# Kernel tuning notes

Hardware: AMD Instinct MI355X
Metric: run time of the kernel (lower is better)

Reference implementation:

```python
import jax, jax.numpy as jnp
import numpy as np
from jax import lax

MD = 4  # max displacement -> 9x9 = 81 correlation channels
NEG_SLOPE = 0.1


def leaky(x):
    return jnp.where(x >= 0, x, NEG_SLOPE * x)


def conv3x3(x, w):
    # NCHW conv, stride 1, padding 1, no bias
    return lax.conv_general_dilated(x, w, (1, 1), 'SAME',
                                    dimension_numbers=('NCHW', 'OIHW', 'NCHW'))


def upsample2x_bilinear(x):
    B, C, H, W = x.shape
    # matches torch F.interpolate(mode='bilinear', align_corners=False)
    return jax.image.resize(x, (B, C, 2 * H, 2 * W), method='bilinear')


def softsplat_average(inp, flow):
    """Forward-warp inp by flow with bilinear splatting, 'average' mode.
    inp: [B,C,H,W], flow: [B,2,H,W] (flow[:,0]=x disp, flow[:,1]=y disp)."""
    B, C, H, W = inp.shape
    val = jnp.concatenate([inp, jnp.ones((B, 1, H, W), inp.dtype)], axis=1)  # [B,C+1,H,W]
    gy, gx = jnp.meshgrid(jnp.arange(H, dtype=inp.dtype), jnp.arange(W, dtype=inp.dtype), indexing='ij')
    fx = gx[None] + flow[:, 0]  # [B,H,W] target x
    fy = gy[None] + flow[:, 1]  # [B,H,W] target y

    x0 = jnp.floor(fx)
    y0 = jnp.floor(fy)
    wx1 = fx - x0
    wy1 = fy - y0
    wx0 = 1.0 - wx1
    wy0 = 1.0 - wy1
    ix0 = x0.astype(jnp.int32)
    iy0 = y0.astype(jnp.int32)

    corners = [(ix0, iy0, wx0 * wy0), (ix0 + 1, iy0, wx1 * wy0),
               (ix0, iy0 + 1, wx0 * wy1), (ix0 + 1, iy0 + 1, wx1 * wy1)]

    def splat_one(val_b, corner_data):
        # val_b: [C+1,H,W]
        v = val_b.reshape(C + 1, H * W)
        out = jnp.zeros((C + 1, H * W), val_b.dtype)
        for ix, iy, w in corner_data:
            valid = (ix >= 0) & (ix < W) & (iy >= 0) & (iy < H)
            idx = jnp.clip(iy, 0, H - 1) * W + jnp.clip(ix, 0, W - 1)
            wv = jnp.where(valid, w, 0.0).reshape(H * W)
            out = out.at[:, idx.reshape(H * W)].add(v * wv[None, :])
        return out.reshape(C + 1, H, W)

    out = jax.vmap(splat_one)(val, [(c[0], c[1], c[2]) for c in corners])
    norm = out[:, -1:]
    norm = jnp.where(norm == 0.0, 1.0, norm)
    return out[:, :-1] / norm


def correlation(f0, f1):
    """PWC-style local cost volume, 9x9 window, mean over channels. [B,81,H,W]."""
    B, C, H, W = f0.shape
    f1p = jnp.pad(f1, ((0, 0), (0, 0), (MD, MD), (MD, MD)))
    vols = []
    for dy in range(2 * MD + 1):
        for dx in range(2 * MD + 1):
            shifted = f1p[:, :, dy:dy + H, dx:dx + W]
            vols.append(jnp.mean(f0 * shifted, axis=1))
    return jnp.stack(vols, axis=1)


def flow_compute(x, W1, W2, W3, W4, W5, W6, W7):
    h = conv3x3(x, W1)
    h = conv3x3(h, W2)
    h = conv3x3(h, W3)
    h = leaky(h)
    h = conv3x3(h, W4)
    h = conv3x3(h, W5)
    h = conv3x3(h, W6)
    h = conv3x3(h, W7)
    return leaky(h)


def setup_inputs() -> dict:
    key = jax.random.key(0)
    ks = jax.random.split(key, 12)
    B, C, H, W = 8, 32, 192, 320
    inp = {
        'feature_0': jax.random.normal(ks[0], (B, C, H, W), jnp.float32),
        'feature_1': jax.random.normal(ks[1], (B, C, H, W), jnp.float32),
        'bi_flow_previous': jax.random.normal(ks[2], (B, 4, H // 2, W // 2), jnp.float32),
        'forward_temporal_feature': jax.random.normal(ks[3], (B, C, H, W), jnp.float32),
        'backward_temporal_feature': jax.random.normal(ks[4], (B, C, H, W), jnp.float32),
        'W1': jax.random.normal(ks[5], (2 * C, 2 * C + 81, 3, 3), jnp.float32) * 0.05,
        'W2': jax.random.normal(ks[6], (2 * C, 2 * C, 3, 3), jnp.float32) * 0.05,
        'W3': jax.random.normal(ks[7], (2 * C, 2 * C, 3, 3), jnp.float32) * 0.05,
        'W4': jax.random.normal(ks[8], (C, 2 * C, 3, 3), jnp.float32) * 0.05,
        'W5': jax.random.normal(ks[9], (C, C, 3, 3), jnp.float32) * 0.05,
        'W6': jax.random.normal(ks[10], (C // 2, C, 3, 3), jnp.float32) * 0.05,
        'W7': jax.random.normal(ks[11], (2, C // 2, 3, 3), jnp.float32) * 0.05,
    }
    return inp


def reference(feature_0, feature_1, bi_flow_previous, forward_temporal_feature,
              backward_temporal_feature, W1, W2, W3, W4, W5, W6, W7):
    bi_flow = upsample2x_bilinear(bi_flow_previous) * 2.0  # [B,4,H,W]
    warped0 = softsplat_average(feature_0, bi_flow[:, :2])
    warped1 = softsplat_average(feature_1, bi_flow[:, 2:])
    volume = leaky(correlation(warped0, warped1))  # [B,81,H,W]
    ws = (W1, W2, W3, W4, W5, W6, W7)
    delta_f = flow_compute(jnp.concatenate([warped0, forward_temporal_feature, volume], axis=1), *ws)
    delta_b = flow_compute(jnp.concatenate([warped1, backward_temporal_feature, volume], axis=1), *ws)
    return bi_flow + jnp.concatenate([delta_f, delta_b], axis=1)
```

## Files before the change

kernel.cpp:

```cpp
#include <hip/hip_runtime.h>

#define IMH 192
#define IMW 320
#define HW_ (IMH * IMW)
#define BB 8
#define FC 32
#define GR 8
#define CCH 224

typedef unsigned short ushortT;
typedef __attribute__((ext_vector_type(8))) short short8;
typedef __attribute__((ext_vector_type(4))) float f32x4;

union FragU { uint4 u; short8 s8; };

__device__ __forceinline__ ushortT f2bf(float x) {
    union { float f; unsigned u; } v; v.f = x;
    unsigned r = v.u + 0x7FFF + ((v.u >> 16) & 1);
    return (ushortT)(r >> 16);
}
__device__ __forceinline__ float lk(float v) { return (v >= 0.f) ? v : 0.1f * v; }

__global__ __launch_bounds__(256) void upsample_k(const float* __restrict__ in,
                                                  float* __restrict__ out) {
    int gid = blockIdx.x * 256 + threadIdx.x;
    const int total = BB * 4 * IMH * IMW;
    if (gid >= total) return;
    int ox = gid % IMW;
    int t  = gid / IMW;
    int oy = t % IMH;
    int bc = t / IMH;
    const int Hin = IMH / 2, Win = IMW / 2;
    float sy = oy * 0.5f - 0.25f;
    float sx = ox * 0.5f - 0.25f;
    float fy = floorf(sy), fx = floorf(sx);
    float ty_ = sy - fy, tx_ = sx - fx;
    int y0 = (int)fy, x0 = (int)fx;
    int y1 = y0 + 1, x1 = x0 + 1;
    y0 = max(0, min(Hin - 1, y0)); y1 = max(0, min(Hin - 1, y1));
    x0 = max(0, min(Win - 1, x0)); x1 = max(0, min(Win - 1, x1));
    const float* p = in + (long)bc * Hin * Win;
    float v00 = p[y0 * Win + x0], v01 = p[y0 * Win + x1];
    float v10 = p[y1 * Win + x0], v11 = p[y1 * Win + x1];
    float v = (1.f - ty_) * ((1.f - tx_) * v00 + tx_ * v01) +
              ty_ * ((1.f - tx_) * v10 + tx_ * v11);
    out[gid] = 2.f * v;
}

__global__ __launch_bounds__(256) void zero4_k(uint4* __restrict__ p, long n) {
    long gid = (long)blockIdx.x * 256 + threadIdx.x;
    long stride = (long)gridDim.x * 256;
    uint4 z = make_uint4(0, 0, 0, 0);
    for (long i = gid; i < n; i += stride) p[i] = z;
}

__global__ __launch_bounds__(256) void trout_k(const float* __restrict__ feat,
                                               const float* __restrict__ biflow,
                                               int fbase,
                                               float* __restrict__ acc,
                                               float* __restrict__ nhwc, int nb) {
    int gid = blockIdx.x * 256 + threadIdx.x;
    if (gid >= nb * HW_) return;
    int b = gid / HW_;
    int p = gid - b * HW_;
    int y = p / IMW, x = p - y * IMW;

    float f[FC];
#pragma unroll
    for (int c = 0; c < FC; ++c) f[c] = feat[((long)b * FC + c) * HW_ + p];
    float4* dst = (float4*)(nhwc + ((long)b * HW_ + p) * FC);
#pragma unroll
    for (int c4 = 0; c4 < FC / 4; ++c4)
        dst[c4] = make_float4(f[c4 * 4 + 0], f[c4 * 4 + 1],
                              f[c4 * 4 + 2], f[c4 * 4 + 3]);

    const float* fl = biflow + ((long)b * 4 + fbase) * HW_;
    float fx = x + fl[p];
    float fy = y + fl[HW_ + p];
    float x0f = floorf(fx), y0f = floorf(fy);
    int ix0 = (int)x0f, iy0 = (int)y0f;
    if (ix0 >= x - GR && ix0 + 1 <= x + GR && iy0 >= y - GR && iy0 + 1 <= y + GR)
        return;
    float wx1 = fx - x0f, wy1 = fy - y0f;
    float wx0 = 1.f - wx1, wy0 = 1.f - wy1;
    float* accb = acc + (long)b * 33 * HW_;
    const int ixs[4] = {ix0, ix0 + 1, ix0, ix0 + 1};
    const int iys[4] = {iy0, iy0, iy0 + 1, iy0 + 1};
    const float ww[4] = {wx0 * wy0, wx1 * wy0, wx0 * wy1, wx1 * wy1};
#pragma unroll
    for (int k = 0; k < 4; ++k) {
        int ix = ixs[k], iy = iys[k];
        float w = ww[k];
        if (ix < 0 || ix >= IMW || iy < 0 || iy >= IMH || w == 0.f) continue;
        int dx = ix - x, dy = iy - y;
        if (dx >= -GR && dx <= GR && dy >= -GR && dy <= GR) continue;
        int q = iy * IMW + ix;
#pragma unroll
        for (int c = 0; c < FC; ++c) atomicAdd(&accb[c * HW_ + q], f[c] * w);
        atomicAdd(&accb[32 * HW_ + q], w);
    }
}

__global__ __launch_bounds__(256) void gather_k(const float* __restrict__ tf0,
                                                const float* __restrict__ tf1,
                                                const float* __restrict__ biflow,
                                                const float* __restrict__ accA,
                                                const float* __restrict__ accB,
                                                ushortT* __restrict__ concat) {
    const int side = blockIdx.z & 1;
    const int b = blockIdx.z >> 1;
    const float* tfeat = side ? tf1 : tf0;
    const float* acc   = side ? accB : accA;
    const int fbase = side ? 2 : 0;
    const int chOff = side ? 160 : 0;

    const int xBase = blockIdx.x * 64;
    const int yBase = blockIdx.y * 4;
    __shared__ float2 sF[20][80];

    const float* fl = biflow + ((long)b * 4 + fbase) * HW_;
    for (int u = threadIdx.x; u < 20 * 80; u += 256) {
        int wy = u / 80, wx = u - wy * 80;
        int gy = yBase - GR + wy, gx = xBase - GR + wx;
        float2 t = make_float2(-1e9f, -1e9f);
        if ((unsigned)gy < IMH && (unsigned)gx < IMW) {
            int p = gy * IMW + gx;
            t.x = gx + fl[p];
            t.y = gy + fl[HW_ + p];
        }
        sF[wy][wx] = t;
    }

    const int lx = threadIdx.x & 63, ly = threadIdx.x >> 6;
    const int ox = xBase + lx, oy = yBase + ly;
    const int q = oy * IMW + ox;
    const float* accb = acc + (long)b * 33 * HW_;

    float s[FC];
#pragma unroll
    for (int c = 0; c < FC; ++c) s[c] = accb[(long)c * HW_ + q];
    float nsum = accb[(long)32 * HW_ + q];

    __syncthreads();

    const float* tb = tfeat + (long)b * HW_ * FC;
    const int pBase = (yBase - GR + ly) * IMW + (xBase - GR + lx);

    for (int dy = 0; dy < 2 * GR + 1; ++dy) {
#pragma unroll 1
        for (int dx = 0; dx < 2 * GR + 1; ++dx) {
            float2 t = sF[ly + dy][lx + dx];
            float x0f = floorf(t.x), y0f = floorf(t.y);
            int dxm = ox - (int)x0f;
            int dym = oy - (int)y0f;
            if (((unsigned)dxm <= 1u) && ((unsigned)dym <= 1u)) {
                float wx1 = t.x - x0f, wy1 = t.y - y0f;
                float w = (dxm ? wx1 : 1.f - wx1) * (dym ? wy1 : 1.f - wy1);
                if (w != 0.f) {
                    nsum += w;
                    int pp = pBase + dy * IMW + dx;
                    const float4* fp = (const float4*)(tb + (long)pp * FC);
#pragma unroll
                    for (int c4 = 0; c4 < FC / 4; ++c4) {
                        float4 v = fp[c4];
                        s[c4 * 4 + 0] = fmaf(w, v.x, s[c4 * 4 + 0]);
                        s[c4 * 4 + 1] = fmaf(w, v.y, s[c4 * 4 + 1]);
                        s[c4 * 4 + 2] = fmaf(w, v.z, s[c4 * 4 + 2]);
                        s[c4 * 4 + 3] = fmaf(w, v.w, s[c4 * 4 + 3]);
                    }
                }
            }
        }
    }

    float inv = (nsum == 0.f) ? 1.f : (1.f / nsum);
    unsigned pk[16];
#pragma unroll
    for (int k = 0; k < 16; ++k) {
        unsigned lo = f2bf(s[2 * k] * inv);
        unsigned hi = f2bf(s[2 * k + 1] * inv);
        pk[k] = lo | (hi << 16);
    }
    uint4* dst = (uint4*)(concat + ((long)b * HW_ + q) * CCH + chOff);
    dst[0] = *(uint4*)&pk[0];
    dst[1] = *(uint4*)&pk[4];
    dst[2] = *(uint4*)&pk[8];
    dst[3] = *(uint4*)&pk[12];
}

__global__ __launch_bounds__(256) void tconv_k(const float* __restrict__ ftf,
                                               const float* __restrict__ btf,
                                               ushortT* __restrict__ concat, int nb) {
    int gid = blockIdx.x * 256 + threadIdx.x;
    if (gid >= nb * HW_ * 8) return;
    int c8 = gid & 7;
    int t = gid >> 3;
    int p = t % HW_;
    int b = t / HW_;
    int ch = c8 * 8;
    const float* src = (ch < 32) ? ftf + ((long)b * 32 + ch) * HW_ + p
                                 : btf + ((long)b * 32 + (ch - 32)) * HW_ + p;
    int chp = (ch < 32) ? (32 + ch) : (192 + (ch - 32));
    ushortT pk[8];
#pragma unroll
    for (int j = 0; j < 8; ++j) pk[j] = f2bf(src[(long)j * HW_]);
    *(uint4*)&concat[((long)b * HW_ + p) * CCH + chp] = *(uint4*)pk;
}

__global__ __launch_bounds__(256) void corr_k(ushortT* __restrict__ concat) {
    const int b = blockIdx.z;
    const int xB = blockIdx.x * 32;
    const int yB = blockIdx.y * 8;
    __shared__ char sW[16 * 40 * 72];

    const long pixBase = (long)b * HW_;

    for (int u = threadIdx.x; u < 16 * 40 * 8; u += 256) {
        int qq = u & 7;
        int site = u >> 3;
        int row = site / 40, col = site - row * 40;
        int gy = yB - 4 + row, gx = xB - 4 + col;
        uint2 v = make_uint2(0u, 0u);
        if ((unsigned)gy < IMH && (unsigned)gx < IMW)
            v = *(const uint2*)(concat + (pixBase + (long)gy * IMW + gx) * CCH + 160 + qq * 4);
        *(uint2*)(sW + site * 72 + qq * 8) = v;
    }

    const int lx = threadIdx.x & 31, ly = threadIdx.x >> 5;
    const int ox = xB + lx, oy = yB + ly;

    unsigned wr[16];
    {
        const uint4* wp = (const uint4*)(concat + (pixBase + (long)oy * IMW + ox) * CCH);
        *(uint4*)&wr[0]  = wp[0];
        *(uint4*)&wr[4]  = wp[1];
        *(uint4*)&wr[8]  = wp[2];
        *(uint4*)&wr[12] = wp[3];
    }
    float w0f[32];
#pragma unroll
    for (int k = 0; k < 16; ++k) {
        union { unsigned u; float f; } lo, hi;
        lo.u = wr[k] << 16;
        hi.u = wr[k] & 0xffff0000u;
        w0f[2 * k]     = lo.f;
        w0f[2 * k + 1] = hi.f;
    }

    __syncthreads();

    const char* lbase = sW + (ly * 40 + lx) * 72;
    unsigned* ob = (unsigned*)concat + (pixBase + (long)oy * IMW + ox) * (CCH / 2) + 32;

    for (int dy = 0; dy < 9; ++dy) {
        const char* rp = lbase + dy * (40 * 72);
        unsigned pd[5] = {0, 0, 0, 0, 0};
#pragma unroll
        for (int dx = 0; dx < 9; ++dx) {
            float s0 = 0.f, s1 = 0.f, s2 = 0.f, s3 = 0.f;
#pragma unroll
            for (int k = 0; k < 8; k += 2) {
                uint2 va = *(const uint2*)(rp + dx * 72 + k * 8);
                uint2 vb = *(const uint2*)(rp + dx * 72 + k * 8 + 8);
                union { unsigned u; float f; } c0, c1, c2, c3, d0, d1, d2, d3;
                c0.u = va.x << 16; c1.u = va.x & 0xffff0000u;
                c2.u = va.y << 16; c3.u = va.y & 0xffff0000u;
                d0.u = vb.x << 16; d1.u = vb.x & 0xffff0000u;
                d2.u = vb.y << 16; d3.u = vb.y & 0xffff0000u;
                s0 = fmaf(w0f[4 * k + 0], c0.f, s0);
                s1 = fmaf(w0f[4 * k + 1], c1.f, s1);
                s2 = fmaf(w0f[4 * k + 2], c2.f, s2);
                s3 = fmaf(w0f[4 * k + 3], c3.f, s3);
                s0 = fmaf(w0f[4 * k + 4], d0.f, s0);
                s1 = fmaf(w0f[4 * k + 5], d1.f, s1);
                s2 = fmaf(w0f[4 * k + 6], d2.f, s2);
                s3 = fmaf(w0f[4 * k + 7], d3.f, s3);
            }
            float s = ((s0 + s1) + (s2 + s3)) * (1.f / 32.f);
            s = lk(s);
            unsigned bf = f2bf(s);
            if (dx & 1) pd[dx >> 1] |= bf << 16;
            else        pd[dx >> 1] = bf;
        }
#pragma unroll
        for (int j = 0; j < 5; ++j) ob[dy * 5 + j] = pd[j];
    }
    ob[45] = 0u; ob[46] = 0u; ob[47] = 0u;
}

__global__ __launch_bounds__(256) void wconv_k(const float* __restrict__ W,
                                               ushortT* __restrict__ dst,
                                               int OC, int OCp, int CIN, int CINp) {
    int gid = blockIdx.x * 256 + threadIdx.x;
    int total = 9 * OCp * CINp;
    if (gid >= total) return;
    int c = gid & 31;
    int t = gid >> 5;
    int oc = t % OCp;
    int t2 = t / OCp;
    int tap = t2 % 9;
    int kc = t2 / 9;
    int cin = kc * 32 + c;
    float v = 0.f;
    if (oc < OC && cin < CIN) v = W[((long)oc * CIN + cin) * 9 + tap];
    dst[gid] = f2bf(v);
}

__global__ __launch_bounds__(256) void wconv1_k(const float* __restrict__ W,
                                                ushortT* __restrict__ dst, int mode) {
    int gid = blockIdx.x * 256 + threadIdx.x;
    const int total = 9 * 64 * 160;
    if (gid >= total) return;
    int c = gid & 31;
    int t = gid >> 5;
    int oc = t % 64;
    int t2 = t / 64;
    int tap = t2 % 9;
    int kc = t2 / 9;
    int cin = kc * 32 + c;
    int src = -1;
    if (mode == 0) {
        if (cin < 64) src = cin;
        else {
            int tt = cin - 64;
            int dy = tt / 10, dx = tt - dy * 10;
            if (dy < 9 && dx < 9) src = 64 + dy * 9 + dx;
        }
    } else {
        if (cin < 96) {
            int dy = cin / 10, dx = cin - dy * 10;
            if (dy < 9 && dx < 9) src = 64 + dy * 9 + dx;
        } else {
            src = cin - 96;
        }
    }
    float v = 0.f;
    if (src >= 0) v = W[((long)oc * 145 + src) * 9 + tap];
    dst[gid] = f2bf(v);
}

template <int MT, int KC, bool LK, bool FIN>
__global__ __launch_bounds__(256) void mconv_k(
    const ushortT* __restrict__ act0, const ushortT* __restrict__ act1, int actStride,
    const ushortT* __restrict__ Wb0, const ushortT* __restrict__ Wb1,
    ushortT* __restrict__ outp0, ushortT* __restrict__ outp1, int outStride,
    const float* __restrict__ bfp, float* __restrict__ fout) {

    const int OCp = MT * 16;
    const int tid = threadIdx.x;
    const int lane = tid & 63;
    const int wv = tid >> 6;
    const int l15 = lane & 15;
    const int quad = lane >> 4;
    const int x0 = blockIdx.x * 32;
    const int y0 = blockIdx.y * 4;
    const int pz = blockIdx.z & 1;
    const int b = blockIdx.z >> 1;

    const ushortT* act = pz ? act1 : act0;
    const ushortT* Wb  = pz ? Wb1  : Wb0;
    ushortT* outp      = pz ? outp1 : outp0;

    __shared__ ushortT sAct[4][6 * 34][8];

    f32x4 acc[MT][2];
#pragma unroll
    for (int i = 0; i < MT; ++i)
#pragma unroll
        for (int j = 0; j < 2; ++j) acc[i][j] = (f32x4)0.f;

    const long pixBase = (long)b * HW_;
    const ushortT* wlane = Wb + (l15 * 32 + quad * 8);

    for (int kc = 0; kc < KC; ++kc) {
        __syncthreads();
        for (int u = tid; u < 6 * 34 * 4; u += 256) {
            int c8 = u & 3;
            int site = u >> 2;
            int ky = site / 34;
            int xi = site - ky * 34;
            int gy = y0 + ky - 1;
            int gx = x0 + xi - 1;
            uint4 v = make_uint4(0, 0, 0, 0);
            if ((unsigned)gy < IMH && (unsigned)gx < IMW)
                v = *(const uint4*)(act + ((pixBase + (long)gy * IMW + gx) * actStride + kc * 32 + c8 * 8));
            *(uint4*)&sAct[c8][site][0] = v;
        }

        const ushortT* wk = wlane + (long)kc * 9 * OCp * 32;
        FragU w0[MT], w1[MT];
#pragma unroll
        for (int mt = 0; mt < MT; ++mt)
            w0[mt].u = *(const uint4*)(wk + mt * 16 * 32);

        __syncthreads();

        FragU b0[2], b1[2];
        {
            const int rowb = wv * 34 + l15;
#pragma unroll
            for (int nt = 0; nt < 2; ++nt)
                b0[nt].u = *(const uint4*)&sAct[quad][rowb + nt * 16][0];
        }

#pragma unroll
        for (int tap = 0; tap < 9; ++tap) {
            FragU* wc = (tap & 1) ? w1 : w0;
            FragU* wn = (tap & 1) ? w0 : w1;
            FragU* bc = (tap & 1) ? b1 : b0;
            FragU* bn = (tap & 1) ? b0 : b1;
            if (tap < 8) {
                const int tap1 = tap + 1;
                const ushortT* wp = wk + tap1 * OCp * 32;
#pragma unroll
                for (int mt = 0; mt < MT; ++mt)
                    wn[mt].u = *(const uint4*)(wp + mt * 16 * 32);
                const int ky = tap1 / 3, kx = tap1 % 3;
                const int rowb = (wv + ky) * 34 + l15 + kx;
#pragma unroll
                for (int nt = 0; nt < 2; ++nt)
                    bn[nt].u = *(const uint4*)&sAct[quad][rowb + nt * 16][0];
            }
#pragma unroll
            for (int mt = 0; mt < MT; ++mt)
#pragma unroll
                for (int nt = 0; nt < 2; ++nt)
                    acc[mt][nt] = __builtin_amdgcn_mfma_f32_16x16x32_bf16(wc[mt].s8, bc[nt].s8, acc[mt][nt], 0, 0, 0);
        }
    }

    const int yo = y0 + wv;
    if (FIN) {
        const int chBase = pz ? 2 : 0;
        if (quad == 0) {
#pragma unroll
            for (int nt = 0; nt < 2; ++nt) {
                int px = x0 + nt * 16 + l15;
#pragma unroll
                for (int r = 0; r < 2; ++r) {
                    float v = lk(acc[0][nt][r]);
                    long o = ((long)(b * 4 + chBase + r) * IMH + yo) * IMW + px;
                    fout[o] = bfp[o] + v;
                }
            }
        }
    } else {
        const long rowBase = (pixBase + (long)yo * IMW) * outStride;
#pragma unroll
        for (int nt = 0; nt < 2; ++nt) {
            long obase = rowBase + (long)(x0 + nt * 16 + l15) * outStride;
#pragma unroll
            for (int mt = 0; mt < MT; ++mt) {
                int oc = mt * 16 + quad * 4;
                ushortT pk[4];
#pragma unroll
                for (int r = 0; r < 4; ++r) {
                    float v = acc[mt][nt][r];
                    if (LK) v = lk(v);
                    pk[r] = f2bf(v);
                }
                *(uint2*)&outp[obase + oc] = *(uint2*)pk;
            }
        }
    }
}

extern "C" void kernel_launch(void* const* d_in, const int* in_sizes, int n_in,
                              void* d_out, int out_size, void* d_ws, size_t ws_size,
                              hipStream_t stream) {
    const float* f0  = (const float*)d_in[0];
    const float* f1  = (const float*)d_in[1];
    const float* bfp = (const float*)d_in[2];
    const float* ftf = (const float*)d_in[3];
    const float* btf = (const float*)d_in[4];
    const float* W1  = (const float*)d_in[5];
    const float* W2  = (const float*)d_in[6];
    const float* W3  = (const float*)d_in[7];
    const float* W4  = (const float*)d_in[8];
    const float* W5  = (const float*)d_in[9];
    const float* W6  = (const float*)d_in[10];
    const float* W7  = (const float*)d_in[11];
    float* out = (float*)d_out;

    char* base = (char*)d_ws;
    size_t off = 0;
    auto alloc = [&](size_t bytes) { char* p = base + off; off += (bytes + 255) & ~(size_t)255; return p; };

    float* biflow = (float*)alloc((size_t)BB * 4 * HW_ * 4);
    ushortT* WbL1a = (ushortT*)alloc((size_t)9 * 64 * 160 * 2);
    ushortT* WbL1b = (ushortT*)alloc((size_t)9 * 64 * 160 * 2);
    ushortT* WbL2 = (ushortT*)alloc((size_t)9 * 64 * 64 * 2);
    ushortT* WbL3 = (ushortT*)alloc((size_t)9 * 64 * 64 * 2);
    ushortT* WbL4 = (ushortT*)alloc((size_t)9 * 32 * 64 * 2);
    ushortT* WbL5 = (ushortT*)alloc((size_t)9 * 32 * 32 * 2);
    ushortT* WbL6 = (ushortT*)alloc((size_t)9 * 16 * 32 * 2);
    ushortT* WbL7 = (ushortT*)alloc((size_t)9 * 16 * 32 * 2);

    const size_t PERB = (size_t)968 * HW_;
    size_t remain = (ws_size > off + 4096) ? (ws_size - off - 4096) : 0;
    int NB = (int)(remain / (PERB + 4096));
    if (NB < 1) NB = 1;
    if (NB > BB) NB = BB;

    float*   acc0   = (float*)alloc((size_t)NB * 33 * HW_ * 4);
    float*   acc1   = (float*)alloc((size_t)NB * 33 * HW_ * 4);
    ushortT* concat = (ushortT*)alloc((size_t)NB * HW_ * CCH * 2);
    ushortT* bufA   = (ushortT*)alloc((size_t)NB * HW_ * 64 * 2);
    ushortT* bufB   = (ushortT*)alloc((size_t)NB * HW_ * 64 * 2);

    ushortT* A1 = (ushortT*)acc0;
    ushortT* B1 = (ushortT*)acc1;

    upsample_k<<<(BB * 4 * HW_ + 255) / 256, 256, 0, stream>>>(bfp, biflow);

    wconv1_k<<<(9 * 64 * 160 + 255) / 256, 256, 0, stream>>>(W1, WbL1a, 0);
    wconv1_k<<<(9 * 64 * 160 + 255) / 256, 256, 0, stream>>>(W1, WbL1b, 1);
    wconv_k<<<(9 * 64 * 64 + 255) / 256, 256, 0, stream>>>(W2, WbL2, 64, 64, 64, 64);
    wconv_k<<<(9 * 64 * 64 + 255) / 256, 256, 0, stream>>>(W3, WbL3, 64, 64, 64, 64);
    wconv_k<<<(9 * 32 * 64 + 255) / 256, 256, 0, stream>>>(W4, WbL4, 32, 32, 64, 64);
    wconv_k<<<(9 * 32 * 32 + 255) / 256, 256, 0, stream>>>(W5, WbL5, 32, 32, 32, 32);
    wconv_k<<<(9 * 16 * 32 + 255) / 256, 256, 0, stream>>>(W6, WbL6, 16, 16, 32, 32);
    wconv_k<<<(9 * 16 * 32 + 255) / 256, 256, 0, stream>>>(W7, WbL7, 2, 16, 16, 32);

    for (int g = 0; g < BB; g += NB) {
        const int nb = (BB - g < NB) ? (BB - g) : NB;
        const int npix = nb * HW_;
        const float* f0g  = f0 + (size_t)g * FC * HW_;
        const float* f1g  = f1 + (size_t)g * FC * HW_;
        const float* ftfg = ftf + (size_t)g * FC * HW_;
        const float* btfg = btf + (size_t)g * FC * HW_;
        const float* bflg = biflow + (size_t)g * 4 * HW_;
        float* outg = out + (size_t)g * 4 * HW_;

        zero4_k<<<2048, 256, 0, stream>>>((uint4*)acc0, (long)NB * 66 * HW_ / 4);

        trout_k<<<(npix + 255) / 256, 256, 0, stream>>>(f0g, bflg, 0, acc0, (float*)bufA, nb);
        trout_k<<<(npix + 255) / 256, 256, 0, stream>>>(f1g, bflg, 2, acc1, (float*)bufB, nb);

        dim3 gg(IMW / 64, IMH / 4, 2 * nb);
        gather_k<<<gg, 256, 0, stream>>>((const float*)bufA, (const float*)bufB,
                                         bflg, acc0, acc1, concat);

        tconv_k<<<(npix * 8 + 255) / 256, 256, 0, stream>>>(ftfg, btfg, concat, nb);

        dim3 cgrid(IMW / 32, IMH / 8, nb);
        corr_k<<<cgrid, 256, 0, stream>>>(concat);

        dim3 cg(10, 48, 2 * nb);
        mconv_k<4, 5, false, false><<<cg, 256, 0, stream>>>(concat, concat + 64, CCH, WbL1a, WbL1b, bufA, A1, 64, nullptr, nullptr);
        mconv_k<4, 2, false, false><<<cg, 256, 0, stream>>>(bufA, A1, 64, WbL2, WbL2, bufB, B1, 64, nullptr, nullptr);
        mconv_k<4, 2, true,  false><<<cg, 256, 0, stream>>>(bufB, B1, 64, WbL3, WbL3, bufA, A1, 64, nullptr, nullptr);
        mconv_k<2, 2, false, false><<<cg, 256, 0, stream>>>(bufA, A1, 64, WbL4, WbL4, bufB, B1, 32, nullptr, nullptr);
        mconv_k<2, 1, false, false><<<cg, 256, 0, stream>>>(bufB, B1, 32, WbL5, WbL5, bufA, A1, 32, nullptr, nullptr);
        mconv_k<1, 1, false, false><<<cg, 256, 0, stream>>>(bufA, A1, 32, WbL6, WbL6, bufB, B1, 16, nullptr, nullptr);
        mconv_k<1, 1, true,  true ><<<cg, 256, 0, stream>>>(bufB, B1, 16, WbL7, WbL7, nullptr, nullptr, 0, bflg, outg);
    }
}
```

Baseline: 1.740 ms.

## Widen conv tile to 64 pixels and stage weights in shared memory

The implicit-GEMM conv kernel now covers 64 pixels per row per block instead of 32, so each wave issues four N-tiles of MFMA per weight fragment. Each K-chunk's weights are loaded cooperatively into padded LDS planes rather than being fetched per lane from global memory with register double-buffering. This raises MFMA work per weight fetch and halves the grid along x. The cost is more LDS use, more accumulator registers and fewer blocks, and activation/weight fragment loads are no longer prefetched across taps.

```diff
diff --git a/kernel.cpp b/kernel.cpp
--- a/kernel.cpp
+++ b/kernel.cpp
@@ -346,13 +346,15 @@
     ushortT* __restrict__ outp0, ushortT* __restrict__ outp1, int outStride,
     const float* __restrict__ bfp, float* __restrict__ fout) {
 
-    const int OCp = MT * 16;
+    constexpr int OCp = MT * 16;
+    constexpr int WPLANE = 9 * OCp * 8 + 8;
+    constexpr int APLANE = 6 * 66 * 8 + 8;
     const int tid = threadIdx.x;
     const int lane = tid & 63;
     const int wv = tid >> 6;
     const int l15 = lane & 15;
     const int quad = lane >> 4;
-    const int x0 = blockIdx.x * 32;
+    const int x0 = blockIdx.x * 64;
     const int y0 = blockIdx.y * 4;
     const int pz = blockIdx.z & 1;
     const int b = blockIdx.z >> 1;
@@ -361,71 +363,59 @@
     const ushortT* Wb  = pz ? Wb1  : Wb0;
     ushortT* outp      = pz ? outp1 : outp0;
 
-    __shared__ ushortT sAct[4][6 * 34][8];
-
-    f32x4 acc[MT][2];
+    __shared__ ushortT sA[4 * APLANE];
+    __shared__ ushortT sW[4 * WPLANE];
+
+    f32x4 acc[MT][4];
 #pragma unroll
     for (int i = 0; i < MT; ++i)
 #pragma unroll
-        for (int j = 0; j < 2; ++j) acc[i][j] = (f32x4)0.f;
+        for (int j = 0; j < 4; ++j) acc[i][j] = (f32x4)0.f;
 
     const long pixBase = (long)b * HW_;
-    const ushortT* wlane = Wb + (l15 * 32 + quad * 8);
 
     for (int kc = 0; kc < KC; ++kc) {
         __syncthreads();
-        for (int u = tid; u < 6 * 34 * 4; u += 256) {
+        for (int u = tid; u < 6 * 66 * 4; u += 256) {
             int c8 = u & 3;
             int site = u >> 2;
-            int ky = site / 34;
-            int xi = site - ky * 34;
+            int ky = site / 66;
+            int xi = site - ky * 66;
             int gy = y0 + ky - 1;
             int gx = x0 + xi - 1;
             uint4 v = make_uint4(0, 0, 0, 0);
             if ((unsigned)gy < IMH && (unsigned)gx < IMW)
                 v = *(const uint4*)(act + ((pixBase + (long)gy * IMW + gx) * actStride + kc * 32 + c8 * 8));
-            *(uint4*)&sAct[c8][site][0] = v;
-        }
-
-        const ushortT* wk = wlane + (long)kc * 9 * OCp * 32;
-        FragU w0[MT], w1[MT];
-#pragma unroll
-        for (int mt = 0; mt < MT; ++mt)
-            w0[mt].u = *(const uint4*)(wk + mt * 16 * 32);
-
+            *(uint4*)&sA[c8 * APLANE + site * 8] = v;
+        }
+        {
+            const ushortT* wk = Wb + (long)kc * 9 * OCp * 32;
+            for (int u = tid; u < 9 * OCp * 4; u += 256) {
+                int c8 = u & 3;
+                int row = u >> 2;
+                *(uint4*)&sW[c8 * WPLANE + row * 8] =
+                    *(const uint4*)(wk + row * 32 + c8 * 8);
+            }
+        }
         __syncthreads();
 
-        FragU b0[2], b1[2];
-        {
-            const int rowb = wv * 34 + l15;
-#pragma unroll
-            for (int nt = 0; nt < 2; ++nt)
-                b0[nt].u = *(const uint4*)&sAct[quad][rowb + nt * 16][0];
-        }
-
 #pragma unroll
         for (int tap = 0; tap < 9; ++tap) {
-            FragU* wc = (tap & 1) ? w1 : w0;
-            FragU* wn = (tap & 1) ? w0 : w1;
-            FragU* bc = (tap & 1) ? b1 : b0;
-            FragU* bn = (tap & 1) ? b0 : b1;
-            if (tap < 8) {
-                const int tap1 = tap + 1;
-                const ushortT* wp = wk + tap1 * OCp * 32;
-#pragma unroll
-                for (int mt = 0; mt < MT; ++mt)
-                    wn[mt].u = *(const uint4*)(wp + mt * 16 * 32);
-                const int ky = tap1 / 3, kx = tap1 % 3;
-                const int rowb = (wv + ky) * 34 + l15 + kx;
-#pragma unroll
-                for (int nt = 0; nt < 2; ++nt)
-                    bn[nt].u = *(const uint4*)&sAct[quad][rowb + nt * 16][0];
-            }
+            const int ky = tap / 3, kx = tap % 3;
+            FragU wf[MT];
 #pragma unroll
             for (int mt = 0; mt < MT; ++mt)
-#pragma unroll
-                for (int nt = 0; nt < 2; ++nt)
-                    acc[mt][nt] = __builtin_amdgcn_mfma_f32_16x16x32_bf16(wc[mt].s8, bc[nt].s8, acc[mt][nt], 0, 0, 0);
+                wf[mt].u = *(const uint4*)&sW[quad * WPLANE + (tap * OCp + mt * 16 + l15) * 8];
+            FragU bf[4];
+            const int rowb = (wv + ky) * 66 + l15 + kx;
+#pragma unroll
+            for (int nt = 0; nt < 4; ++nt)
+                bf[nt].u = *(const uint4*)&sA[quad * APLANE + (rowb + nt * 16) * 8];
+#pragma unroll
+            for (int mt = 0; mt < MT; ++mt)
+#pragma unroll
+                for (int nt = 0; nt < 4; ++nt)
+                    acc[mt][nt] = __builtin_amdgcn_mfma_f32_16x16x32_bf16(wf[mt].s8, bf[nt].s8, acc[mt][nt], 0, 0, 0);
         }
     }
 
@@ -434,7 +424,7 @@
         const int chBase = pz ? 2 : 0;
         if (quad == 0) {
 #pragma unroll
-            for (int nt = 0; nt < 2; ++nt) {
+            for (int nt = 0; nt < 4; ++nt) {
                 int px = x0 + nt * 16 + l15;
 #pragma unroll
                 for (int r = 0; r < 2; ++r) {
@@ -447,7 +437,7 @@
     } else {
         const long rowBase = (pixBase + (long)yo * IMW) * outStride;
 #pragma unroll
-        for (int nt = 0; nt < 2; ++nt) {
+        for (int nt = 0; nt < 4; ++nt) {
             long obase = rowBase + (long)(x0 + nt * 16 + l15) * outStride;
 #pragma unroll
             for (int mt = 0; mt < MT; ++mt) {
@@ -546,7 +536,7 @@
         dim3 cgrid(IMW / 32, IMH / 8, nb);
         corr_k<<<cgrid, 256, 0, stream>>>(concat);
 
-        dim3 cg(10, 48, 2 * nb);
+        dim3 cg(5, 48, 2 * nb);
         mconv_k<4, 5, false, false><<<cg, 256, 0, stream>>>(concat, concat + 64, CCH, WbL1a, WbL1b, bufA, A1, 64, nullptr, nullptr);
         mconv_k<4, 2, false, false><<<cg, 256, 0, stream>>>(bufA, A1, 64, WbL2, WbL2, bufB, B1, 64, nullptr, nullptr);
         mconv_k<4, 2, true,  false><<<cg, 256, 0, stream>>>(bufB, B1, 64, WbL3, WbL3, bufA, A1, 64, nullptr, nullptr);
```

Result: faster. 1.543 ms (-11.4%).
